# Kernel tuning notes

Measured on AMD Instinct MI355X. Metric: run time of the kernel, lower is better.

The kernel has to match this reference:

```python
import jax, jax.numpy as jnp
import numpy as np

NEG_INF = -1e10  # masked_fill value from the torch module


def setup_inputs() -> dict:
    key = jax.random.key(0)
    k1, k2, k3, k4, k5 = jax.random.split(key, 5)
    B, S, H = 64, 2048, 512
    return {
        "decoder_hidden": jax.random.normal(k1, (B, H), dtype=jnp.float32),
        "encoder_outputs": jax.random.normal(k2, (B, S, 2 * H), dtype=jnp.float32),
        "mask": jnp.ones((B, S), dtype=jnp.int32),
        "Wd": jax.random.normal(k3, (H, H), dtype=jnp.float32) * (1.0 / np.sqrt(H)),
        "We": jax.random.normal(k4, (2 * H, H), dtype=jnp.float32) * (1.0 / np.sqrt(2 * H)),
        "v": jax.random.normal(k5, (H,), dtype=jnp.float32) * (1.0 / np.sqrt(H)),
    }


def reference(decoder_hidden, encoder_outputs, mask, Wd, We, v):
    # decoder_proj: (B, H); encoder_proj: (B, S, H)
    dec_proj = decoder_hidden @ Wd
    enc_proj = jnp.einsum("bse,eh->bsh", encoder_outputs, We)
    energy = jnp.tanh(dec_proj[:, None, :] + enc_proj)  # (B, S, H)
    scores = jnp.einsum("bsh,h->bs", energy, v)  # (B, S)
    scores = jnp.where(mask == 0, NEG_INF, scores)
    attn_weights = jax.nn.softmax(scores, axis=1)  # (B, S)
    context = jnp.einsum("bs,bsd->bd", attn_weights, encoder_outputs)  # (B, 2H)
    return (context, attn_weights)
```

## Files before the change

### kernel.cpp

```cpp
#include <hip/hip_runtime.h>

typedef _Float16 f16;
typedef f16  f16x4 __attribute__((ext_vector_type(4)));
typedef f16  f16x8 __attribute__((ext_vector_type(8)));
typedef float f32x4 __attribute__((ext_vector_type(4)));

#define B_  64
#define S_  2048
#define H_  512
#define K_  1024

__device__ __forceinline__ float fast_tanh(float x){
  float ax = fabsf(x);
  float t  = __expf(-2.0f*ax);
  float r  = (1.0f - t) / (1.0f + t);
  return x < 0.0f ? -r : r;
}

__global__ __launch_bounds__(256) void prep_k(const float* __restrict__ We,
                                              f16* __restrict__ Bg,
                                              const float* __restrict__ dh,
                                              const float* __restrict__ Wd,
                                              float* __restrict__ dp,
                                              const float* __restrict__ vvg,
                                              float* __restrict__ vC){
  __shared__ float s_dh[512];
  if (blockIdx.x < 2048){
    int idx = blockIdx.x*256 + threadIdx.x;
    int k = idx >> 9, col = idx & 511;
    Bg[((k>>3)<<12) + (col<<3) + (k&7)] = (f16)We[idx];
  } else if (blockIdx.x < 2176){
    int idx = blockIdx.x - 2048;
    int b = idx >> 1, cg = idx & 1;
    int col = (cg<<8) + threadIdx.x;
    for (int i = threadIdx.x; i < 512; i += 256) s_dh[i] = dh[(b<<9) + i];
    __syncthreads();
    float a0=0.f,a1=0.f,a2=0.f,a3=0.f;
    for (int k = 0; k < 512; k += 4){
      a0 += s_dh[k+0]*Wd[(k+0)*512 + col];
      a1 += s_dh[k+1]*Wd[(k+1)*512 + col];
      a2 += s_dh[k+2]*Wd[(k+2)*512 + col];
      a3 += s_dh[k+3]*Wd[(k+3)*512 + col];
    }
    dp[(b<<9) + col] = (a0+a1)+(a2+a3);
  } else {
    int t = threadIdx.x;
    float a = fabsf(vvg[t]) + fabsf(vvg[t+256]);
    #pragma unroll
    for (int o = 32; o >= 1; o >>= 1) a += __shfl_xor(a, o);
    if ((t & 63) == 0) s_dh[t>>6] = a;
    __syncthreads();
    if (t == 0) vC[0] = s_dh[0]+s_dh[1]+s_dh[2]+s_dh[3];
  }
}

__global__ __launch_bounds__(512, 2) void fused_k(
    const float* __restrict__ enc,
    const f16*   __restrict__ Bg,
    const float* __restrict__ dp,
    const float* __restrict__ vvg,
    const float* __restrict__ vC,
    const int*   __restrict__ mask,
    float*       __restrict__ pbuf,
    float*       __restrict__ denom,
    float*       __restrict__ part)
{
  __shared__ __align__(16) f16 At[2][2048];
  __shared__ __align__(16) f16 Bt[2][16384];
  __shared__ float s_sc[64];

  const int tid  = threadIdx.x;
  const int lane = tid & 63;
  const int wave = tid >> 6;
  const int b    = blockIdx.x >> 5;
  const int s0   = (blockIdx.x & 31) << 6;

  if (tid < 64) s_sc[tid] = 0.0f;

  const int arow = tid >> 3;
  const int akq  = tid & 7;
  const int kgrp = akq >> 1, apar = akq & 1;
  const float* aG = enc + ((size_t)(b*S_ + s0 + arow) << 10) + (akq << 2);
  const int aDst = (kgrp<<9) + ((arow ^ (kgrp<<1))<<3) + (apar<<2);

  const int r16 = lane & 15, g = lane >> 4;
  const int aFrag = (g<<9) + ((r16 ^ (g<<1))<<3);
  const int colb  = wave << 6;

  f32x4 acc[4][4] = {};

  auto stageB = [&](int buf, int kt){
    const f16* srcBase = Bg + ((size_t)kt << 14);
    #pragma unroll
    for (int gg = 0; gg < 4; ++gg){
      int off = (gg<<12) + (colb<<3) + (lane<<3);
      __builtin_amdgcn_global_load_lds(
          (const __attribute__((address_space(1))) void*)(srcBase + off),
          (__attribute__((address_space(3))) void*)(&Bt[buf][off]),
          16, 0, 0);
    }
  };
  auto loadA = [&](int t)->f32x4 { return *(const f32x4*)(aG + (t<<5)); };
  auto putA  = [&](f32x4 a4, int buf){
    f16x4 h4; h4[0]=(f16)a4[0]; h4[1]=(f16)a4[1]; h4[2]=(f16)a4[2]; h4[3]=(f16)a4[3];
    *(f16x4*)&At[buf][aDst] = h4;
  };

  stageB(0, 0);
  f32x4 a0 = loadA(0);
  stageB(1, 1);
  f32x4 aCur = loadA(1);
  putA(a0, 0);
  asm volatile("s_waitcnt lgkmcnt(0)" ::: "memory");
  __builtin_amdgcn_sched_barrier(0);
  __builtin_amdgcn_s_barrier();
  __builtin_amdgcn_sched_barrier(0);

  for (int t = 0; t < 32; ++t){
    const int cur = t & 1;
    if (t < 31){
      stageB(cur^1, t+1);
      f32x4 aNext = loadA(t+2 <= 31 ? t+2 : 31);
      putA(aCur, cur^1);
      aCur = aNext;
    } else {
      asm volatile("s_waitcnt vmcnt(1)" ::: "memory");
      __builtin_amdgcn_sched_barrier(0);
    }
    f16x8 af[4], bfr[4];
    #pragma unroll
    for (int n = 0; n < 4; ++n)
      bfr[n] = *(const f16x8*)&Bt[cur][(g<<12) + ((colb + (n<<4) + r16)<<3)];
    #pragma unroll
    for (int m = 0; m < 4; ++m)
      af[m] = *(const f16x8*)&At[cur][aFrag + (m<<7)];
    __builtin_amdgcn_s_setprio(1);
    #pragma unroll
    for (int m = 0; m < 4; ++m)
      #pragma unroll
      for (int n = 0; n < 4; ++n)
        acc[m][n] = __builtin_amdgcn_mfma_f32_16x16x32_f16(af[m], bfr[n], acc[m][n], 0, 0, 0);
    __builtin_amdgcn_s_setprio(0);
    if (t < 31){
      asm volatile("s_waitcnt lgkmcnt(0)" ::: "memory");
      __builtin_amdgcn_sched_barrier(0);
      __builtin_amdgcn_s_barrier();
      __builtin_amdgcn_sched_barrier(0);
    }
  }

  float dpv[4], vvv[4];
  #pragma unroll
  for (int n = 0; n < 4; ++n){
    int c = colb + (n<<4) + r16;
    dpv[n] = dp[(b<<9) + c];
    vvv[n] = vvg[c];
  }
  float sp[4][4];
  #pragma unroll
  for (int m = 0; m < 4; ++m)
    #pragma unroll
    for (int r = 0; r < 4; ++r) sp[m][r] = 0.f;
  #pragma unroll
  for (int m = 0; m < 4; ++m)
    #pragma unroll
    for (int n = 0; n < 4; ++n)
      #pragma unroll
      for (int r = 0; r < 4; ++r){
        float e = fast_tanh(acc[m][n][r] + dpv[n]);
        sp[m][r] += vvv[n]*e;
      }
  #pragma unroll
  for (int m = 0; m < 4; ++m)
    #pragma unroll
    for (int r = 0; r < 4; ++r){
      float x = sp[m][r];
      x += __shfl_xor(x, 1);
      x += __shfl_xor(x, 2);
      x += __shfl_xor(x, 4);
      x += __shfl_xor(x, 8);
      if (r16 == 0) atomicAdd(&s_sc[(m<<4) + (g<<2) + r], x);
    }
  __syncthreads();

  const float C = vC[0];
  if (tid < 64){
    float s = s_sc[tid];
    int mk = mask[(b<<11) + s0 + tid];
    float p = mk ? __expf(s - C) : 0.0f;
    s_sc[tid] = p;
    pbuf[(b<<11) + s0 + tid] = p;
    float d = p;
    #pragma unroll
    for (int o = 32; o >= 1; o >>= 1) d += __shfl_xor(d, o);
    if (tid == 0) denom[(b<<5) + (blockIdx.x & 31)] = d;
  }
  __syncthreads();

  {
    const float2* e2 = (const float2*)(enc + ((size_t)(b*S_ + s0) << 10)) + tid;
    float ax = 0.f, ay = 0.f;
    #pragma unroll 4
    for (int s = 0; s < 64; ++s){
      float w = s_sc[s];
      float2 x = e2[s*512];
      ax += w * x.x; ay += w * x.y;
    }
    float2* pp = (float2*)part + ((size_t)blockIdx.x << 9) + tid;
    *pp = make_float2(ax, ay);
  }
}

__global__ __launch_bounds__(256) void combine_k(const float* __restrict__ part,
                                                 const float* __restrict__ denom,
                                                 const float* __restrict__ pbuf,
                                                 float* __restrict__ ctx,
                                                 float* __restrict__ attn){
  const int b = blockIdx.x, tid = threadIdx.x;
  float D = 0.f;
  #pragma unroll
  for (int c = 0; c < 32; ++c) D += denom[(b<<5) + c];
  D = fmaxf(D, 1e-37f);
  const float inv = 1.0f / D;

  f32x4 acc = {0.f,0.f,0.f,0.f};
  const f32x4* p4 = (const f32x4*)part;
  #pragma unroll
  for (int c = 0; c < 32; ++c)
    acc += p4[(((b<<5)+c)<<8) + tid];
  ((f32x4*)ctx)[(b<<8) + tid] = acc * inv;

  #pragma unroll
  for (int i = 0; i < 8; ++i){
    int s = tid + (i<<8);
    attn[(b<<11) + s] = pbuf[(b<<11) + s] * inv;
  }
}

extern "C" void kernel_launch(void* const* d_in, const int* in_sizes, int n_in,
                              void* d_out, int out_size, void* d_ws, size_t ws_size,
                              hipStream_t stream){
  (void)in_sizes; (void)n_in; (void)out_size;
  const size_t WS_NEED = 1712384u + 8388608u;
  if (ws_size < WS_NEED) return;

  const float* dec_h = (const float*)d_in[0];
  const float* enc   = (const float*)d_in[1];
  const int*   mask  = (const int*)d_in[2];
  const float* Wd    = (const float*)d_in[3];
  const float* We    = (const float*)d_in[4];
  const float* v     = (const float*)d_in[5];
  float* out  = (float*)d_out;
  float* ctx  = out;
  float* attn = out + B_*2*H_;

  char* ws = (char*)d_ws;
  f16*   Bg     = (f16*)ws;
  float* dproj  = (float*)(ws + 1048576);
  float* vC     = (float*)(ws + 1179648);
  float* pbuf   = (float*)(ws + 1179904);
  float* denom  = (float*)(ws + 1704192);
  float* part   = (float*)(ws + 1712384);

  prep_k   <<<2177, 256, 0, stream>>>(We, Bg, dec_h, Wd, dproj, v, vC);
  fused_k  <<<2048, 512, 0, stream>>>(enc, Bg, dproj, v, vC, mask, pbuf, denom, part);
  combine_k<<<B_, 256, 0, stream>>>(part, denom, pbuf, ctx, attn);
}
```

Measured before the change: 301.0 us.

## Load B fragments directly from global instead of staging through LDS

Removes the double-buffered LDS staging of the fp16 We tile (global_load_lds) and has each wave read its B fragments straight from global/L2 into registers each k-step. This cuts LDS usage per block from about 72KB to about 8KB, which could raise occupancy and removes the B-side LDS traffic. It also reorders the A prefetch and loads A fragments per m inside the MFMA loop. In exchange, B loads are no longer prefetched a step ahead, so global latency sits on the critical path and each wave re-reads B from cache.

```diff
diff --git a/kernel.cpp b/kernel.cpp
--- a/kernel.cpp
+++ b/kernel.cpp
@@ -66,7 +66,6 @@
     float*       __restrict__ part)
 {
   __shared__ __align__(16) f16 At[2][2048];
-  __shared__ __align__(16) f16 Bt[2][16384];
   __shared__ float s_sc[64];
 
   const int tid  = threadIdx.x;
@@ -87,30 +86,21 @@
   const int aFrag = (g<<9) + ((r16 ^ (g<<1))<<3);
   const int colb  = wave << 6;
 
+  const f16* bP = Bg + (g<<12) + ((colb + r16)<<3);
+
   f32x4 acc[4][4] = {};
 
-  auto stageB = [&](int buf, int kt){
-    const f16* srcBase = Bg + ((size_t)kt << 14);
-    #pragma unroll
-    for (int gg = 0; gg < 4; ++gg){
-      int off = (gg<<12) + (colb<<3) + (lane<<3);
-      __builtin_amdgcn_global_load_lds(
-          (const __attribute__((address_space(1))) void*)(srcBase + off),
-          (__attribute__((address_space(3))) void*)(&Bt[buf][off]),
-          16, 0, 0);
-    }
-  };
   auto loadA = [&](int t)->f32x4 { return *(const f32x4*)(aG + (t<<5)); };
   auto putA  = [&](f32x4 a4, int buf){
     f16x4 h4; h4[0]=(f16)a4[0]; h4[1]=(f16)a4[1]; h4[2]=(f16)a4[2]; h4[3]=(f16)a4[3];
     *(f16x4*)&At[buf][aDst] = h4;
   };
 
-  stageB(0, 0);
-  f32x4 a0 = loadA(0);
-  stageB(1, 1);
+  {
+    f32x4 a0 = loadA(0);
+    putA(a0, 0);
+  }
   f32x4 aCur = loadA(1);
-  putA(a0, 0);
   asm volatile("s_waitcnt lgkmcnt(0)" ::: "memory");
   __builtin_amdgcn_sched_barrier(0);
   __builtin_amdgcn_s_barrier();
@@ -118,35 +108,34 @@
 
   for (int t = 0; t < 32; ++t){
     const int cur = t & 1;
+    f32x4 aNext;
     if (t < 31){
-      stageB(cur^1, t+1);
-      f32x4 aNext = loadA(t+2 <= 31 ? t+2 : 31);
       putA(aCur, cur^1);
-      aCur = aNext;
-    } else {
-      asm volatile("s_waitcnt vmcnt(1)" ::: "memory");
-      __builtin_amdgcn_sched_barrier(0);
-    }
-    f16x8 af[4], bfr[4];
+    }
+    f16x8 bfr[4];
     #pragma unroll
     for (int n = 0; n < 4; ++n)
-      bfr[n] = *(const f16x8*)&Bt[cur][(g<<12) + ((colb + (n<<4) + r16)<<3)];
-    #pragma unroll
-    for (int m = 0; m < 4; ++m)
-      af[m] = *(const f16x8*)&At[cur][aFrag + (m<<7)];
+      bfr[n] = *(const f16x8*)(bP + (n<<7));
+    if (t < 31){
+      aNext = loadA(t+2 <= 31 ? t+2 : 31);
+    }
     __builtin_amdgcn_s_setprio(1);
     #pragma unroll
-    for (int m = 0; m < 4; ++m)
+    for (int m = 0; m < 4; ++m){
+      f16x8 af = *(const f16x8*)&At[cur][aFrag + (m<<7)];
       #pragma unroll
       for (int n = 0; n < 4; ++n)
-        acc[m][n] = __builtin_amdgcn_mfma_f32_16x16x32_f16(af[m], bfr[n], acc[m][n], 0, 0, 0);
+        acc[m][n] = __builtin_amdgcn_mfma_f32_16x16x32_f16(af, bfr[n], acc[m][n], 0, 0, 0);
+    }
     __builtin_amdgcn_s_setprio(0);
     if (t < 31){
       asm volatile("s_waitcnt lgkmcnt(0)" ::: "memory");
       __builtin_amdgcn_sched_barrier(0);
       __builtin_amdgcn_s_barrier();
       __builtin_amdgcn_sched_barrier(0);
-    }
+      aCur = aNext;
+    }
+    bP += (1<<14);
   }
 
   float dpv[4], vvv[4];
```

After: 288.0 us (median of 2 runs). 4.3% less time.
